# Performance work log

Measured on AMD Instinct MI355X. Metric: run time of the kernel, lower is better.

Reference implementation:

```python
import jax, jax.numpy as jnp
import numpy as np

HEAD = 16
HEAD_DIM = 64
DIM = 1024
NEG = -1000000000.0


def setup_inputs() -> dict:
    key = jax.random.key(0)
    ks = jax.random.split(key, 8)
    B, S = 4, 2048
    s = 0.02
    return {
        "Q": jax.random.normal(ks[0], (B, S, DIM), dtype=jnp.float32),
        "K": jax.random.normal(ks[1], (B, S, DIM), dtype=jnp.float32),
        "V": jax.random.normal(ks[2], (B, S, DIM), dtype=jnp.float32),
        "Wq": jax.random.normal(ks[3], (HEAD * HEAD_DIM, DIM), dtype=jnp.float32) * s,
        "Wk": jax.random.normal(ks[4], (HEAD * HEAD_DIM, DIM), dtype=jnp.float32) * s,
        "Wv": jax.random.normal(ks[5], (HEAD * HEAD_DIM, DIM), dtype=jnp.float32) * s,
        "Wo": jax.random.normal(ks[6], (DIM, HEAD * HEAD_DIM), dtype=jnp.float32) * s,
        "bo": jax.random.normal(ks[7], (DIM,), dtype=jnp.float32) * s,
    }


def reference(Q, K, V, Wq, Wk, Wv, Wo, bo):
    B, S, _ = Q.shape
    # projections (nn.Linear: x @ W^T), split heads -> (b, h, t, d)
    def proj(x, W):
        return (x @ W.T).reshape(B, S, HEAD, HEAD_DIM).transpose(0, 2, 1, 3)
    q = proj(Q, Wq)
    k = proj(K, Wk)
    v = proj(V, Wv)
    scores = jnp.einsum("bhqd,bhkd->bhqk", q, k) / jnp.sqrt(jnp.float32(HEAD_DIM))
    causal = jnp.tril(jnp.ones((S, S), dtype=bool))
    scores = jnp.where(causal, scores, NEG)
    weights = jax.nn.softmax(scores, axis=-1)
    out = jnp.einsum("bhqk,bhkd->bhqd", weights, v)
    out = out.transpose(0, 2, 1, 3).reshape(B, S, HEAD * HEAD_DIM)
    out = out @ Wo.T + bo
    return out, weights
```

## Files before the change

kernel.cpp:

```cpp
#include <hip/hip_runtime.h>
#include <hip/hip_bf16.h>

typedef __hip_bfloat16 bf16;
typedef __attribute__((ext_vector_type(8))) short bf16x8;
typedef __attribute__((ext_vector_type(4))) float f32x4;

#define HEADS 16
#define HDIM  64
#define DIM   1024
#define SEQ   2048
#define BATCH 4
#define BS    (BATCH * SEQ)
#define CS    0.1803368801111f

#define EXP2F(x) __builtin_amdgcn_exp2f(x)
#define LOG2F(x) __builtin_amdgcn_logf(x)
#define MFMA16(a, b, c) __builtin_amdgcn_mfma_f32_16x16x32_bf16(a, b, c, 0, 0, 0)

__device__ __forceinline__ void gload_lds16(const void* g, void* l) {
    __builtin_amdgcn_global_load_lds(
        (const __attribute__((address_space(1))) void*)g,
        (__attribute__((address_space(3))) void*)l, 16, 0, 0);
}

__device__ __forceinline__ void cvt8(const float* __restrict__ src, bf16* __restrict__ dst,
                                     size_t i)
{
    float4 f0 = *(const float4*)&src[i];
    float4 f1 = *(const float4*)&src[i + 4];
    union { bf16 h[8]; uint4 u; } pk;
    pk.h[0] = __float2bfloat16(f0.x); pk.h[1] = __float2bfloat16(f0.y);
    pk.h[2] = __float2bfloat16(f0.z); pk.h[3] = __float2bfloat16(f0.w);
    pk.h[4] = __float2bfloat16(f1.x); pk.h[5] = __float2bfloat16(f1.y);
    pk.h[6] = __float2bfloat16(f1.z); pk.h[7] = __float2bfloat16(f1.w);
    *(uint4*)&dst[i] = pk.u;
}

__global__ __launch_bounds__(256) void cvt_kernel(
    const float* __restrict__ Q, const float* __restrict__ K, const float* __restrict__ V,
    const float* __restrict__ Wq, const float* __restrict__ Wk, const float* __restrict__ Wv,
    bf16* __restrict__ xq, bf16* __restrict__ xk, bf16* __restrict__ xv,
    bf16* __restrict__ wq, bf16* __restrict__ wk, bf16* __restrict__ wv)
{
    const int seg = blockIdx.y;
    const float* src; bf16* dst; size_t n;
    switch (seg) {
        case 0: src = Q;  dst = xq; n = (size_t)BS * DIM;   break;
        case 1: src = K;  dst = xk; n = (size_t)BS * DIM;   break;
        case 2: src = V;  dst = xv; n = (size_t)BS * DIM;   break;
        case 3: src = Wq; dst = wq; n = (size_t)DIM * DIM;  break;
        case 4: src = Wk; dst = wk; n = (size_t)DIM * DIM;  break;
        default: src = Wv; dst = wv; n = (size_t)DIM * DIM; break;
    }
    size_t i = ((size_t)blockIdx.x * 256 + threadIdx.x) * 8;
    if (i >= n) return;
    cvt8(src, dst, i);
}

__global__ __launch_bounds__(256) void cvt_wo_kernel(
    const float* __restrict__ Wo, bf16* __restrict__ wo)
{
    size_t i = ((size_t)blockIdx.x * 256 + threadIdx.x) * 8;
    cvt8(Wo, wo, i);
}

template <bool SWAP>
__device__ __forceinline__ void mfma_core_1024(
    const bf16* __restrict__ A, const bf16* __restrict__ B,
    int m0, int n0, bf16* sA, f32x4 acc[4][4])
{
    const int tid = threadIdx.x, lane = tid & 63, wave = tid >> 6;
    const int l15 = lane & 15, lg = lane >> 4;
    const int wr = wave >> 1, wc = wave & 1;
    bf16* sB = sA + 16 * 512;

    const bf16* gsrc = (wave < 2) ? A : B;
    const int   gm0  = (wave < 2) ? m0 : n0;
    bf16*       sdst = (wave < 2) ? sA : sB;
    const int   wv2  = wave & 1;

#define STAGE(k0_) { \
    _Pragma("unroll") for (int u = 0; u < 8; ++u) { \
        const int c = wv2 * 8 + u; \
        const int mg = c >> 1, s = c & 1; \
        gload_lds16(gsrc + (size_t)(gm0 + mg * 16 + l15) * DIM + (k0_) + s * 32 + lg * 8, \
                    sdst + c * 512); \
    } }

    STAGE(0);
#pragma unroll 1
    for (int t = 0; t < DIM / 64; ++t) {
        __syncthreads();
#pragma unroll
        for (int s = 0; s < 2; ++s) {
            bf16x8 af[4], bfr[4];
#pragma unroll
            for (int i = 0; i < 4; ++i)
                af[i] = *(const bf16x8*)(sA + ((wr * 4 + i) * 2 + s) * 512 + lane * 8);
#pragma unroll
            for (int j = 0; j < 4; ++j)
                bfr[j] = *(const bf16x8*)(sB + ((wc * 4 + j) * 2 + s) * 512 + lane * 8);
#pragma unroll
            for (int i = 0; i < 4; ++i)
#pragma unroll
                for (int j = 0; j < 4; ++j) {
                    if (SWAP) acc[i][j] = MFMA16(bfr[j], af[i], acc[i][j]);
                    else      acc[i][j] = MFMA16(af[i], bfr[j], acc[i][j]);
                }
        }
        __syncthreads();
        if (t < DIM / 64 - 1) STAGE((t + 1) * 64);
    }
#undef STAGE
}

__global__ __launch_bounds__(256) void proj_mfma_kernel(
    const bf16* __restrict__ Xq, const bf16* __restrict__ Xk, const bf16* __restrict__ Xv,
    const bf16* __restrict__ Wq, const bf16* __restrict__ Wk, const bf16* __restrict__ Wv,
    bf16* __restrict__ qo, bf16* __restrict__ ko, bf16* __restrict__ vo)
{
    __shared__ alignas(16) bf16 smem[16384];
    const int z = blockIdx.z;
    const bf16* X = z == 0 ? Xq : z == 1 ? Xk : Xv;
    const bf16* W = z == 0 ? Wq : z == 1 ? Wk : Wv;
    const int m0 = blockIdx.y * 128, n0 = blockIdx.x * 128;

    const int tid = threadIdx.x, lane = tid & 63, wave = tid >> 6;
    const int l15 = lane & 15, lg = lane >> 4, wr = wave >> 1, wc = wave & 1;
    const int h = blockIdx.x * 2 + wc;

    f32x4 acc[4][4] = {};
    if (z != 2) {
        mfma_core_1024<true>(X, W, m0, n0, smem, acc);
        const float osc = (z == 0) ? CS : 1.0f;
        bf16* O = z == 0 ? qo : ko;
#pragma unroll
        for (int i = 0; i < 4; ++i) {
            int m = m0 + wr * 64 + i * 16 + l15;
            int bb = m >> 11, ss = m & (SEQ - 1);
            size_t base = ((size_t)(bb * HEADS + h) * SEQ + ss) * HDIM;
#pragma unroll
            for (int j = 0; j < 4; ++j) {
                union { bf16 h4[4]; uint2 u; } pk;
#pragma unroll
                for (int r = 0; r < 4; ++r) pk.h4[r] = __float2bfloat16(acc[i][j][r] * osc);
                *(uint2*)&O[base + j * 16 + lg * 4] = pk.u;
            }
        }
    } else {
        mfma_core_1024<false>(X, W, m0, n0, smem, acc);
#pragma unroll
        for (int i = 0; i < 4; ++i) {
            int s0 = m0 + wr * 64 + i * 16 + lg * 4;
            int bb = s0 >> 11, ss = s0 & (SEQ - 1);
#pragma unroll
            for (int j = 0; j < 4; ++j) {
                int d = j * 16 + l15;
                union { bf16 h4[4]; uint2 u; } pk;
#pragma unroll
                for (int r = 0; r < 4; ++r) pk.h4[r] = __float2bfloat16(acc[i][j][r]);
                *(uint2*)&vo[((size_t)(bb * HEADS + h) * HDIM + d) * SEQ + ss] = pk.u;
            }
        }
    }
}

__global__ __launch_bounds__(256) void attn_kernel(
    const bf16* __restrict__ qws, const bf16* __restrict__ kws, const bf16* __restrict__ vtws,
    float* __restrict__ weights, bf16* __restrict__ attn_out)
{
    __shared__ alignas(16) bf16 Ks[4096];
    __shared__ alignas(16) bf16 Vs[4096];
    __shared__ alignas(16) bf16 Ps[4096];

    const int tid  = threadIdx.x;
    const int lane = tid & 63;
    const int wave = tid >> 6;
    const int l15  = lane & 15;
    const int lg   = lane >> 4;
    const int qt = (int)gridDim.x - 1 - (int)blockIdx.x;
    const int h  = blockIdx.y, b = blockIdx.z;
    const int bh = b * HEADS + h;
    const int q0 = qt * 64;
    const int qloc = 16 * wave + l15;

    const bf16* qbase = qws + (size_t)bh * SEQ * HDIM;
    const bf16* kbase = kws + (size_t)bh * SEQ * HDIM;
    const bf16* vbase = vtws + (size_t)bh * HDIM * SEQ;

    bf16x8 qa0, qa1;
    {
        const bf16* qp = qbase + (size_t)(q0 + qloc) * HDIM + lg * 8;
        qa0 = *(const bf16x8*)qp;
        qa1 = *(const bf16x8*)(qp + 32);
    }

#define LOADK(kt_, r0, r1) { \
    const bf16* rp = kbase + (size_t)((kt_) * 64 + 16 * wave + l15) * HDIM + lg * 8; \
    r0 = *(const uint4*)rp; r1 = *(const uint4*)(rp + 32); }
#define STOREK(r0, r1) { \
    *(uint4*)&Ks[((wave * 2 + 0) * 64 + lane) * 8] = r0; \
    *(uint4*)&Ks[((wave * 2 + 1) * 64 + lane) * 8] = r1; }
#define LOADV(kt_, r0, r1) { \
    const bf16* rp = vbase + (size_t)(16 * wave + l15) * SEQ + (kt_) * 64 + lg * 8; \
    r0 = *(const uint4*)rp; r1 = *(const uint4*)(rp + 32); }
#define STOREV(r0, r1) { \
    *(uint4*)&Vs[((wave * 2 + 0) * 64 + lane) * 8] = r0; \
    *(uint4*)&Vs[((wave * 2 + 1) * 64 + lane) * 8] = r1; }
#define QKT(acc_) { \
    _Pragma("unroll") \
    for (int ct = 0; ct < 4; ++ct) { \
        bf16x8 b0 = *(const bf16x8*)&Ks[((ct * 2 + 0) * 64 + lane) * 8]; \
        bf16x8 b1 = *(const bf16x8*)&Ks[((ct * 2 + 1) * 64 + lane) * 8]; \
        acc_[ct] = MFMA16(b0, qa0, acc_[ct]); \
        acc_[ct] = MFMA16(b1, qa1, acc_[ct]); \
    } }

    float l_run = 0.f;

    {
        uint4 k0, k1;
        LOADK(0, k0, k1);
        STOREK(k0, k1);
    }
    for (int kt = 0; kt <= qt; ++kt) {
        __syncthreads();
        f32x4 acc[4] = {};
        QKT(acc);
        const bool more = kt < qt;
        uint4 nk0, nk1;
        if (more) LOADK(kt + 1, nk0, nk1);
        const bool diag = (kt == qt);
        float ps = 0.f;
#pragma unroll
        for (int ct = 0; ct < 4; ++ct)
#pragma unroll
            for (int r = 0; r < 4; ++r) {
                float v = acc[ct][r];
                if (diag && (ct * 16 + lg * 4 + r > qloc)) v = -1e30f;
                ps += EXP2F(v);
            }
        ps += __shfl_xor(ps, 16);
        ps += __shfl_xor(ps, 32);
        l_run += ps;
        __syncthreads();
        if (more) STOREK(nk0, nk1);
    }

    const float lg2il = -LOG2F(l_run);

    {
        uint4 k0, k1, v0, v1;
        LOADK(0, k0, k1);
        LOADV(0, v0, v1);
        STOREK(k0, k1);
        STOREV(v0, v1);
    }
    f32x4 oacc[4] = {};
    const size_t wrow = ((size_t)bh * SEQ + q0 + qloc) * SEQ;

    for (int kt = 0; kt <= qt; ++kt) {
        __syncthreads();
        f32x4 acc[4] = {};
        QKT(acc);
        const bool more = kt < qt;
        uint4 nk0, nk1, nv0, nv1;
        if (more) { LOADK(kt + 1, nk0, nk1); LOADV(kt + 1, nv0, nv1); }
        const bool diag = (kt == qt);
#pragma unroll
        for (int ct = 0; ct < 4; ++ct) {
            f32x4 w4;
            union { bf16 h4[4]; uint2 u; } pk;
#pragma unroll
            for (int r = 0; r < 4; ++r) {
                float v = acc[ct][r];
                if (diag && (ct * 16 + lg * 4 + r > qloc)) v = -1e30f;
                float w = EXP2F(v + lg2il);
                w4[r] = w;
                pk.h4[r] = __float2bfloat16(w);
            }
            __builtin_nontemporal_store(
                w4, (f32x4*)&weights[wrow + kt * 64 + ct * 16 + lg * 4]);
            *(uint2*)&Ps[(((wave * 2 + (ct >> 1)) * 64
                           + ((ct & 1) * 2 + (lg >> 1)) * 16 + l15) * 8
                          + (lg & 1) * 4)] = pk.u;
        }
        bf16x8 pa0 = *(const bf16x8*)&Ps[((wave * 2 + 0) * 64 + lane) * 8];
        bf16x8 pa1 = *(const bf16x8*)&Ps[((wave * 2 + 1) * 64 + lane) * 8];
#pragma unroll
        for (int td = 0; td < 4; ++td) {
            bf16x8 vb0 = *(const bf16x8*)&Vs[((td * 2 + 0) * 64 + lane) * 8];
            bf16x8 vb1 = *(const bf16x8*)&Vs[((td * 2 + 1) * 64 + lane) * 8];
            oacc[td] = MFMA16(vb0, pa0, oacc[td]);
            oacc[td] = MFMA16(vb1, pa1, oacc[td]);
        }
        __syncthreads();
        if (more) { STOREK(nk0, nk1); STOREV(nv0, nv1); }
    }

    {
        const size_t obase = ((size_t)b * SEQ + q0 + 16 * wave + l15) * DIM
                           + h * HDIM + lg * 4;
#pragma unroll
        for (int td = 0; td < 4; ++td) {
            union { bf16 h4[4]; uint2 u; } pk;
#pragma unroll
            for (int r = 0; r < 4; ++r) pk.h4[r] = __float2bfloat16(oacc[td][r]);
            *(uint2*)&attn_out[obase + td * 16] = pk.u;
        }
    }

    const int zc0 = (qt + 1) * 64;
    if (zc0 < SEQ) {
        const int nc4 = (SEQ - zc0) >> 2;
        const size_t base = ((size_t)bh * SEQ + q0) * SEQ + zc0;
        const f32x4 z = {0.f, 0.f, 0.f, 0.f};
        for (int r = 0; r < 64; ++r)
            for (int c = tid; c < nc4; c += 256)
                __builtin_nontemporal_store(
                    z, (f32x4*)&weights[base + (size_t)r * SEQ + (size_t)c * 4]);
    }
#undef LOADK
#undef STOREK
#undef LOADV
#undef STOREV
#undef QKT
}

__global__ __launch_bounds__(256) void oproj_mfma_kernel(
    const bf16* __restrict__ A, const bf16* __restrict__ Wo,
    const float* __restrict__ bo, float* __restrict__ out)
{
    __shared__ alignas(16) bf16 smem[16384];
    const int m0 = blockIdx.y * 128, n0 = blockIdx.x * 128;
    f32x4 acc[4][4] = {};
    mfma_core_1024<true>(A, Wo, m0, n0, smem, acc);

    const int tid = threadIdx.x, lane = tid & 63, wave = tid >> 6;
    const int l15 = lane & 15, lg = lane >> 4, wr = wave >> 1, wc = wave & 1;
    f32x4 bv[4];
#pragma unroll
    for (int j = 0; j < 4; ++j)
        bv[j] = *(const f32x4*)&bo[n0 + wc * 64 + j * 16 + lg * 4];
#pragma unroll
    for (int i = 0; i < 4; ++i) {
        int m = m0 + wr * 64 + i * 16 + l15;
#pragma unroll
        for (int j = 0; j < 4; ++j) {
            f32x4 v = acc[i][j] + bv[j];
            *(f32x4*)&out[(size_t)m * DIM + n0 + wc * 64 + j * 16 + lg * 4] = v;
        }
    }
}

extern "C" void kernel_launch(void* const* d_in, const int* in_sizes, int n_in,
                              void* d_out, int out_size, void* d_ws, size_t ws_size,
                              hipStream_t stream)
{
    const float* Q  = (const float*)d_in[0];
    const float* K  = (const float*)d_in[1];
    const float* V  = (const float*)d_in[2];
    const float* Wq = (const float*)d_in[3];
    const float* Wk = (const float*)d_in[4];
    const float* Wv = (const float*)d_in[5];
    const float* Wo = (const float*)d_in[6];
    const float* bo = (const float*)d_in[7];

    float* out     = (float*)d_out;
    float* weights = out + (size_t)BS * DIM;

    const size_t XN = (size_t)BS * DIM;
    const size_t WN = (size_t)DIM * DIM;
    const size_t scratch_elems = 3 * XN + 3 * WN;
    bf16* cvt = (bf16*)(weights + ((size_t)268435456 - scratch_elems / 2));
    bf16* xq  = cvt;
    bf16* xk  = xq + XN;
    bf16* xv  = xk + XN;
    bf16* wqc = xv + XN;
    bf16* wkc = wqc + WN;
    bf16* wvc = wkc + WN;

    bf16* qws  = (bf16*)d_ws;
    bf16* kws  = qws + (size_t)BS * DIM;
    bf16* vtws = kws + (size_t)BS * DIM;
    bf16* aws  = vtws + (size_t)BS * DIM;
    bf16* woc  = qws;

    dim3 blk(256);
    cvt_kernel<<<dim3(4096, 6), blk, 0, stream>>>(
        Q, K, V, Wq, Wk, Wv, xq, xk, xv, wqc, wkc, wvc);
    proj_mfma_kernel<<<dim3(DIM / 128, BS / 128, 3), blk, 0, stream>>>(
        xq, xk, xv, wqc, wkc, wvc, qws, kws, vtws);
    attn_kernel<<<dim3(SEQ / 64, HEADS, BATCH), blk, 0, stream>>>(
        qws, kws, vtws, weights, aws);
    cvt_wo_kernel<<<dim3(WN / (256 * 8)), blk, 0, stream>>>(Wo, woc);
    oproj_mfma_kernel<<<dim3(DIM / 128, BS / 128), blk, 0, stream>>>(
        aws, woc, bo, out);
}
```

Baseline: 490.1 us.

## Process 128 query rows per attention block to reuse K/V tiles

Result: slower. 536.4 us (+9.5%).

```diff
diff --git a/kernel.cpp b/kernel.cpp
--- a/kernel.cpp
+++ b/kernel.cpp
@@ -12,6 +12,7 @@
 #define BATCH 4
 #define BS    (BATCH * SEQ)
 #define CS    0.1803368801111f
+#define QBLK  128
 
 #define EXP2F(x) __builtin_amdgcn_exp2f(x)
 #define LOG2F(x) __builtin_amdgcn_logf(x)
@@ -171,7 +172,7 @@
 {
     __shared__ alignas(16) bf16 Ks[4096];
     __shared__ alignas(16) bf16 Vs[4096];
-    __shared__ alignas(16) bf16 Ps[4096];
+    __shared__ alignas(16) bf16 Ps[8192];
 
     const int tid  = threadIdx.x;
     const int lane = tid & 63;
@@ -181,18 +182,21 @@
     const int qt = (int)gridDim.x - 1 - (int)blockIdx.x;
     const int h  = blockIdx.y, b = blockIdx.z;
     const int bh = b * HEADS + h;
-    const int q0 = qt * 64;
-    const int qloc = 16 * wave + l15;
+    const int q0 = qt * QBLK;
+    const int qlA = 32 * wave + l15;
+    const int nkt = 2 * qt + 2;
 
     const bf16* qbase = qws + (size_t)bh * SEQ * HDIM;
     const bf16* kbase = kws + (size_t)bh * SEQ * HDIM;
     const bf16* vbase = vtws + (size_t)bh * HDIM * SEQ;
 
-    bf16x8 qa0, qa1;
+    bf16x8 qa0A, qa1A, qa0B, qa1B;
     {
-        const bf16* qp = qbase + (size_t)(q0 + qloc) * HDIM + lg * 8;
-        qa0 = *(const bf16x8*)qp;
-        qa1 = *(const bf16x8*)(qp + 32);
+        const bf16* qp = qbase + (size_t)(q0 + qlA) * HDIM + lg * 8;
+        qa0A = *(const bf16x8*)qp;
+        qa1A = *(const bf16x8*)(qp + 32);
+        qa0B = *(const bf16x8*)(qp + 16 * HDIM);
+        qa1B = *(const bf16x8*)(qp + 16 * HDIM + 32);
     }
 
 #define LOADK(kt_, r0, r1) { \
@@ -207,47 +211,53 @@
 #define STOREV(r0, r1) { \
     *(uint4*)&Vs[((wave * 2 + 0) * 64 + lane) * 8] = r0; \
     *(uint4*)&Vs[((wave * 2 + 1) * 64 + lane) * 8] = r1; }
-#define QKT(acc_) { \
+#define QKT2(accA_, accB_) { \
     _Pragma("unroll") \
     for (int ct = 0; ct < 4; ++ct) { \
         bf16x8 b0 = *(const bf16x8*)&Ks[((ct * 2 + 0) * 64 + lane) * 8]; \
         bf16x8 b1 = *(const bf16x8*)&Ks[((ct * 2 + 1) * 64 + lane) * 8]; \
-        acc_[ct] = MFMA16(b0, qa0, acc_[ct]); \
-        acc_[ct] = MFMA16(b1, qa1, acc_[ct]); \
+        accA_[ct] = MFMA16(b0, qa0A, accA_[ct]); \
+        accA_[ct] = MFMA16(b1, qa1A, accA_[ct]); \
+        accB_[ct] = MFMA16(b0, qa0B, accB_[ct]); \
+        accB_[ct] = MFMA16(b1, qa1B, accB_[ct]); \
     } }
 
-    float l_run = 0.f;
+    float lA = 0.f, lB = 0.f;
 
     {
         uint4 k0, k1;
         LOADK(0, k0, k1);
         STOREK(k0, k1);
     }
-    for (int kt = 0; kt <= qt; ++kt) {
-        __syncthreads();
-        f32x4 acc[4] = {};
-        QKT(acc);
-        const bool more = kt < qt;
+    for (int kt = 0; kt < nkt; ++kt) {
+        __syncthreads();
+        f32x4 accA[4] = {}, accB[4] = {};
+        QKT2(accA, accB);
+        const bool more = kt + 1 < nkt;
         uint4 nk0, nk1;
         if (more) LOADK(kt + 1, nk0, nk1);
-        const bool diag = (kt == qt);
-        float ps = 0.f;
+        const int dA = q0 + qlA - kt * 64;
+        float psA = 0.f, psB = 0.f;
 #pragma unroll
         for (int ct = 0; ct < 4; ++ct)
 #pragma unroll
             for (int r = 0; r < 4; ++r) {
-                float v = acc[ct][r];
-                if (diag && (ct * 16 + lg * 4 + r > qloc)) v = -1e30f;
-                ps += EXP2F(v);
+                const int e = ct * 16 + lg * 4 + r;
+                psA += EXP2F(e > dA      ? -1e30f : accA[ct][r]);
+                psB += EXP2F(e > dA + 16 ? -1e30f : accB[ct][r]);
             }
-        ps += __shfl_xor(ps, 16);
-        ps += __shfl_xor(ps, 32);
-        l_run += ps;
+        psA += __shfl_xor(psA, 16);
+        psA += __shfl_xor(psA, 32);
+        psB += __shfl_xor(psB, 16);
+        psB += __shfl_xor(psB, 32);
+        lA += psA;
+        lB += psB;
         __syncthreads();
         if (more) STOREK(nk0, nk1);
     }
 
-    const float lg2il = -LOG2F(l_run);
+    const float lg2ilA = -LOG2F(lA);
+    const float lg2ilB = -LOG2F(lB);
 
     {
         uint4 k0, k1, v0, v1;
@@ -256,66 +266,81 @@
         STOREK(k0, k1);
         STOREV(v0, v1);
     }
-    f32x4 oacc[4] = {};
-    const size_t wrow = ((size_t)bh * SEQ + q0 + qloc) * SEQ;
-
-    for (int kt = 0; kt <= qt; ++kt) {
-        __syncthreads();
-        f32x4 acc[4] = {};
-        QKT(acc);
-        const bool more = kt < qt;
+    f32x4 oA[4] = {}, oB[4] = {};
+    const size_t wrowA = ((size_t)bh * SEQ + q0 + qlA) * SEQ;
+    const size_t wrowB = wrowA + (size_t)16 * SEQ;
+
+    for (int kt = 0; kt < nkt; ++kt) {
+        __syncthreads();
+        f32x4 accA[4] = {}, accB[4] = {};
+        QKT2(accA, accB);
+        const bool more = kt + 1 < nkt;
         uint4 nk0, nk1, nv0, nv1;
         if (more) { LOADK(kt + 1, nk0, nk1); LOADV(kt + 1, nv0, nv1); }
-        const bool diag = (kt == qt);
+        const int dA = q0 + qlA - kt * 64;
 #pragma unroll
         for (int ct = 0; ct < 4; ++ct) {
-            f32x4 w4;
-            union { bf16 h4[4]; uint2 u; } pk;
+            f32x4 wA, wB;
+            union { bf16 h4[4]; uint2 u; } pkA, pkB;
 #pragma unroll
             for (int r = 0; r < 4; ++r) {
-                float v = acc[ct][r];
-                if (diag && (ct * 16 + lg * 4 + r > qloc)) v = -1e30f;
-                float w = EXP2F(v + lg2il);
-                w4[r] = w;
-                pk.h4[r] = __float2bfloat16(w);
+                const int e = ct * 16 + lg * 4 + r;
+                float a = EXP2F((e > dA      ? -1e30f : accA[ct][r]) + lg2ilA);
+                float c = EXP2F((e > dA + 16 ? -1e30f : accB[ct][r]) + lg2ilB);
+                wA[r] = a; pkA.h4[r] = __float2bfloat16(a);
+                wB[r] = c; pkB.h4[r] = __float2bfloat16(c);
             }
             __builtin_nontemporal_store(
-                w4, (f32x4*)&weights[wrow + kt * 64 + ct * 16 + lg * 4]);
-            *(uint2*)&Ps[(((wave * 2 + (ct >> 1)) * 64
-                           + ((ct & 1) * 2 + (lg >> 1)) * 16 + l15) * 8
-                          + (lg & 1) * 4)] = pk.u;
-        }
-        bf16x8 pa0 = *(const bf16x8*)&Ps[((wave * 2 + 0) * 64 + lane) * 8];
-        bf16x8 pa1 = *(const bf16x8*)&Ps[((wave * 2 + 1) * 64 + lane) * 8];
+                wA, (f32x4*)&weights[wrowA + kt * 64 + ct * 16 + lg * 4]);
+            __builtin_nontemporal_store(
+                wB, (f32x4*)&weights[wrowB + kt * 64 + ct * 16 + lg * 4]);
+            const int sub = ((ct & 1) * 2 + (lg >> 1)) * 16 + l15;
+            *(uint2*)&Ps[(((wave * 4 + 0 + (ct >> 1)) * 64) + sub) * 8 + (lg & 1) * 4]
+                = pkA.u;
+            *(uint2*)&Ps[(((wave * 4 + 2 + (ct >> 1)) * 64) + sub) * 8 + (lg & 1) * 4]
+                = pkB.u;
+        }
+        bf16x8 paA0 = *(const bf16x8*)&Ps[(wave * 4 + 0) * 512 + lane * 8];
+        bf16x8 paA1 = *(const bf16x8*)&Ps[(wave * 4 + 1) * 512 + lane * 8];
+        bf16x8 paB0 = *(const bf16x8*)&Ps[(wave * 4 + 2) * 512 + lane * 8];
+        bf16x8 paB1 = *(const bf16x8*)&Ps[(wave * 4 + 3) * 512 + lane * 8];
 #pragma unroll
         for (int td = 0; td < 4; ++td) {
             bf16x8 vb0 = *(const bf16x8*)&Vs[((td * 2 + 0) * 64 + lane) * 8];
             bf16x8 vb1 = *(const bf16x8*)&Vs[((td * 2 + 1) * 64 + lane) * 8];
-            oacc[td] = MFMA16(vb0, pa0, oacc[td]);
-            oacc[td] = MFMA16(vb1, pa1, oacc[td]);
+            oA[td] = MFMA16(vb0, paA0, oA[td]);
+            oA[td] = MFMA16(vb1, paA1, oA[td]);
+            oB[td] = MFMA16(vb0, paB0, oB[td]);
+            oB[td] = MFMA16(vb1, paB1, oB[td]);
         }
         __syncthreads();
         if (more) { STOREK(nk0, nk1); STOREV(nv0, nv1); }
     }
 
     {
-        const size_t obase = ((size_t)b * SEQ + q0 + 16 * wave + l15) * DIM
-                           + h * HDIM + lg * 4;
+        const size_t obase = ((size_t)b * SEQ + q0 + qlA) * DIM + h * HDIM + lg * 4;
 #pragma unroll
         for (int td = 0; td < 4; ++td) {
             union { bf16 h4[4]; uint2 u; } pk;
 #pragma unroll
-            for (int r = 0; r < 4; ++r) pk.h4[r] = __float2bfloat16(oacc[td][r]);
+            for (int r = 0; r < 4; ++r) pk.h4[r] = __float2bfloat16(oA[td][r]);
             *(uint2*)&attn_out[obase + td * 16] = pk.u;
         }
-    }
-
-    const int zc0 = (qt + 1) * 64;
+#pragma unroll
+        for (int td = 0; td < 4; ++td) {
+            union { bf16 h4[4]; uint2 u; } pk;
+#pragma unroll
+            for (int r = 0; r < 4; ++r) pk.h4[r] = __float2bfloat16(oB[td][r]);
+            *(uint2*)&attn_out[obase + (size_t)16 * DIM + td * 16] = pk.u;
+        }
+    }
+
+    const int zc0 = (qt + 1) * QBLK;
     if (zc0 < SEQ) {
         const int nc4 = (SEQ - zc0) >> 2;
         const size_t base = ((size_t)bh * SEQ + q0) * SEQ + zc0;
         const f32x4 z = {0.f, 0.f, 0.f, 0.f};
-        for (int r = 0; r < 64; ++r)
+        for (int r = 0; r < QBLK; ++r)
             for (int c = tid; c < nc4; c += 256)
                 __builtin_nontemporal_store(
                     z, (f32x4*)&weights[base + (size_t)r * SEQ + (size_t)c * 4]);
@@ -324,7 +349,7 @@
 #undef STOREK
 #undef LOADV
 #undef STOREV
-#undef QKT
+#undef QKT2
 }
 
 __global__ __launch_bounds__(256) void oproj_mfma_kernel(
@@ -391,7 +416,7 @@
         Q, K, V, Wq, Wk, Wv, xq, xk, xv, wqc, wkc, wvc);
     proj_mfma_kernel<<<dim3(DIM / 128, BS / 128, 3), blk, 0, stream>>>(
         xq, xk, xv, wqc, wkc, wvc, qws, kws, vtws);
-    attn_kernel<<<dim3(SEQ / 64, HEADS, BATCH), blk, 0, stream>>>(
+    attn_kernel<<<dim3(SEQ / QBLK, HEADS, BATCH), blk, 0, stream>>>(
         qws, kws, vtws, weights, aws);
     cvt_wo_kernel<<<dim3(WN / (256 * 8)), blk, 0, stream>>>(Wo, woc);
     oproj_mfma_kernel<<<dim3(DIM / 128, BS / 128), blk, 0, stream>>>(
```
